# Kernel optimization log

Measured on AMD Instinct MI355X. Metric: run time of the kernel, lower is better.

Reference implementation:

```python
import jax, jax.numpy as jnp
import numpy as np

B, S, D = 4, 4096, 1024
E, H, TOPK = 8, 2752, 2


def setup_inputs() -> dict:
    key = jax.random.key(0)
    k0, k1, k2, k3, k4 = jax.random.split(key, 5)
    x = jax.random.normal(k0, (B, S, D), dtype=jnp.float32)
    gate_w = jax.random.normal(k1, (E, D), dtype=jnp.float32) * 0.02
    w1 = jax.random.normal(k2, (E, H, D), dtype=jnp.float32) * 0.02
    w2 = jax.random.normal(k3, (E, D, H), dtype=jnp.float32) * 0.02
    w3 = jax.random.normal(k4, (E, H, D), dtype=jnp.float32) * 0.02
    return {"x": x, "gate_w": gate_w, "w1": w1, "w2": w2, "w3": w3}


def reference(x, gate_w, w1, w2, w3):
    """MoE layer: softmax router -> top-k (normalized) -> per-expert SwiGLU FFN -> weighted combine."""
    b, s, d = x.shape
    xt = x.reshape(-1, d)                       # [T, D], T = B*S
    logits = xt @ gate_w.T                      # [T, E]
    scores = jax.nn.softmax(logits, axis=-1)
    topk_w, topk_i = jax.lax.top_k(scores, TOPK)  # [T, K]
    topk_w = topk_w / (jnp.sum(topk_w, axis=-1, keepdims=True) + 1e-20)

    y = jnp.zeros_like(xt)
    n_experts = gate_w.shape[0]
    for e in range(n_experts):
        # combine weight for expert e per token (0 if not routed to e)
        we = jnp.sum(jnp.where(topk_i == e, topk_w, 0.0), axis=-1)  # [T]
        h = jax.nn.silu(xt @ w1[e].T) * (xt @ w3[e].T)              # [T, H]
        y = y + we[:, None] * (h @ w2[e].T)                         # [T, D]
    return y.reshape(b, s, d)
```

## Files before the change

kernel.cpp:

```cpp
#include <hip/hip_runtime.h>
#include <hip/hip_bf16.h>
#include <stdint.h>

#define T_TOK 16384
#define D_DIM 1024
#define E_NUM 8
#define H_DIM 2752
#define NSLOT (T_TOK * 2)

typedef __bf16 bf16x8_t __attribute__((ext_vector_type(8)));
typedef float f32x4_t __attribute__((ext_vector_type(4)));
typedef float f32x16_t __attribute__((ext_vector_type(16)));

__device__ __forceinline__ uint16_t f2bf(float f) {
    union { float f; uint32_t u; } v; v.f = f;
    return (uint16_t)((v.u + 0x7FFFu + ((v.u >> 16) & 1u)) >> 16);
}
__device__ __forceinline__ ushort4 f4_to_bf4(float4 v) {
    ushort4 r; r.x = f2bf(v.x); r.y = f2bf(v.y); r.z = f2bf(v.z); r.w = f2bf(v.w);
    return r;
}
__device__ __forceinline__ void gl_lds16(const uint16_t* g, uint16_t* l) {
    __builtin_amdgcn_global_load_lds((const __attribute__((address_space(1))) void*)g,
                                     (__attribute__((address_space(3))) void*)l,
                                     16, 0, 0);
}

__global__ __launch_bounds__(256) void router_kernel(
    const float* __restrict__ x, const float* __restrict__ gw,
    int* __restrict__ topk_i, float* __restrict__ topk_w,
    uint16_t* __restrict__ Xb) {
    int tid = threadIdx.x;
    int t = blockIdx.x * 4 + (tid >> 6);
    int lane = tid & 63;
    const float* xr = x + (size_t)t * D_DIM;
    double acc[E_NUM];
#pragma unroll
    for (int e = 0; e < E_NUM; ++e) acc[e] = 0.0;
    for (int k = lane; k < D_DIM; k += 64) {
        double xv = (double)xr[k];
#pragma unroll
        for (int e = 0; e < E_NUM; ++e) acc[e] += xv * (double)gw[e * D_DIM + k];
    }
    {
        const float4* x4 = (const float4*)xr;
        ushort4* b4 = (ushort4*)(Xb + (size_t)t * D_DIM);
#pragma unroll
        for (int j = 0; j < 4; ++j) b4[lane + j * 64] = f4_to_bf4(x4[lane + j * 64]);
    }
#pragma unroll
    for (int e = 0; e < E_NUM; ++e) {
        double v = acc[e];
        for (int off = 32; off > 0; off >>= 1) v += __shfl_down(v, off, 64);
        acc[e] = v;
    }
    if (lane == 0) {
        int i0 = 0; double m0 = acc[0];
#pragma unroll
        for (int e = 1; e < E_NUM; ++e) if (acc[e] > m0) { m0 = acc[e]; i0 = e; }
        int i1 = -1; double m1 = -1.0e300;
#pragma unroll
        for (int e = 0; e < E_NUM; ++e) if (e != i0 && acc[e] > m1) { m1 = acc[e]; i1 = e; }
        double e1 = exp(m1 - m0);
        double s = 1.0 + e1;
        topk_i[t * 2 + 0] = i0; topk_i[t * 2 + 1] = i1;
        topk_w[t * 2 + 0] = (float)(1.0 / s);
        topk_w[t * 2 + 1] = (float)(e1 / s);
    }
}

__global__ __launch_bounds__(256) void count_kernel(
    const int* __restrict__ topk_i,
    int* __restrict__ counts_f, int* __restrict__ counts_s) {
    __shared__ int hf[E_NUM], hs[E_NUM];
    int tid = threadIdx.x;
    if (tid < E_NUM) { hf[tid] = 0; hs[tid] = 0; }
    __syncthreads();
    int t = blockIdx.x * 256 + tid;
    atomicAdd(&hf[topk_i[t * 2 + 0]], 1);
    atomicAdd(&hs[topk_i[t * 2 + 1]], 1);
    __syncthreads();
    if (tid < E_NUM) {
        if (hf[tid]) atomicAdd(&counts_f[tid], hf[tid]);
    } else if (tid < 2 * E_NUM) {
        int e = tid - E_NUM;
        if (hs[e]) atomicAdd(&counts_s[e], hs[e]);
    }
}

__global__ void prefix_kernel(const int* __restrict__ cf, const int* __restrict__ cs,
                              int* __restrict__ bases, int* __restrict__ splits,
                              int* __restrict__ cnts) {
    int s = 0;
    for (int e = 0; e < E_NUM; ++e) {
        bases[e] = s;
        splits[e] = s + cf[e];
        cnts[e] = cf[e] + cs[e];
        s += cnts[e];
    }
}

__global__ __launch_bounds__(256) void assign_kernel(
    const int* __restrict__ topk_i, const float* __restrict__ topk_w,
    const int* __restrict__ bases, const int* __restrict__ splits,
    int* __restrict__ fills_f, int* __restrict__ fills_s,
    int* __restrict__ slot_tok, float* __restrict__ slot_w) {
    __shared__ int hf[E_NUM], hs[E_NUM], bf[E_NUM], bs[E_NUM];
    int tid = threadIdx.x;
    if (tid < E_NUM) { hf[tid] = 0; hs[tid] = 0; }
    __syncthreads();
    int t = blockIdx.x * 256 + tid;
    int e0 = topk_i[t * 2 + 0], e1 = topk_i[t * 2 + 1];
    int r0 = atomicAdd(&hf[e0], 1);
    int r1 = atomicAdd(&hs[e1], 1);
    __syncthreads();
    if (tid < E_NUM) {
        bf[tid] = hf[tid] ? atomicAdd(&fills_f[tid], hf[tid]) : 0;
    } else if (tid < 2 * E_NUM) {
        int e = tid - E_NUM;
        bs[e] = hs[e] ? atomicAdd(&fills_s[e], hs[e]) : 0;
    }
    __syncthreads();
    int s0 = bases[e0] + bf[e0] + r0;
    int s1 = splits[e1] + bs[e1] + r1;
    slot_tok[s0] = t; slot_w[s0] = topk_w[t * 2 + 0];
    slot_tok[s1] = t; slot_w[s1] = topk_w[t * 2 + 1];
}

__global__ __launch_bounds__(256) void cvt13g_kernel(const float* __restrict__ w1,
                                                     const float* __restrict__ w3,
                                                     uint16_t* __restrict__ w1be,
                                                     uint16_t* __restrict__ w3be, int g) {
    size_t i = (size_t)blockIdx.x * 256 + threadIdx.x;
    size_t off = (size_t)g * 4 * H_DIM * D_DIM / 4;
    ((ushort4*)w1be)[i] = f4_to_bf4(((const float4*)w1)[off + i]);
    ((ushort4*)w3be)[i] = f4_to_bf4(((const float4*)w3)[off + i]);
}
__global__ __launch_bounds__(256) void cvt2_kernel(const float* __restrict__ w2,
                                                   uint16_t* __restrict__ w2b) {
    size_t i = (size_t)blockIdx.x * 256 + threadIdx.x;
    ((ushort4*)w2b)[i] = f4_to_bf4(((const float4*)w2)[i]);
}


__global__ __launch_bounds__(256) void gemm1_kernel(
    const uint16_t* __restrict__ Xb, const uint16_t* __restrict__ w1be,
    const uint16_t* __restrict__ w3be, const int* __restrict__ slot_tok,
    const int* __restrict__ cnts, const int* __restrict__ bases,
    uint16_t* __restrict__ hidden, int g) {
    int ez = blockIdx.z;
    int e = g * 4 + ez;
    int cnt = cnts[e];
    int m0 = blockIdx.y * 128;
    if (m0 >= cnt) return;
    int n0 = blockIdx.x * 64;
    int base = bases[e];
    const uint16_t* w1p = w1be + (size_t)ez * H_DIM * D_DIM;
    const uint16_t* w3p = w3be + (size_t)ez * H_DIM * D_DIM;

    __shared__ __align__(16) uint16_t As[128 * 64];
    __shared__ __align__(16) uint16_t B1s[64 * 64];
    __shared__ __align__(16) uint16_t B3s[64 * 64];

    int tid = threadIdx.x;
    int w = tid >> 6, lane = tid & 63;
    int l31 = lane & 31, khi = lane >> 5;
    int r8 = lane >> 3;
    int srcc = (lane & 7) ^ ((w * 4 + (lane >> 4)) & 7);
    int xr2 = (l31 >> 1) & 7;

    const uint16_t *pA0, *pA1, *pA2, *pA3, *pB1, *pB3;
    {
        int sr = w * 8 + r8;
        int t0 = slot_tok[base + min(m0 + 0 * 32 + sr, cnt - 1)];
        int t1 = slot_tok[base + min(m0 + 1 * 32 + sr, cnt - 1)];
        int t2 = slot_tok[base + min(m0 + 2 * 32 + sr, cnt - 1)];
        int t3 = slot_tok[base + min(m0 + 3 * 32 + sr, cnt - 1)];
        pA0 = Xb + (size_t)t0 * D_DIM + srcc * 8;
        pA1 = Xb + (size_t)t1 * D_DIM + srcc * 8;
        pA2 = Xb + (size_t)t2 * D_DIM + srcc * 8;
        pA3 = Xb + (size_t)t3 * D_DIM + srcc * 8;
        pB1 = w1p + (size_t)(n0 + sr) * D_DIM + srcc * 8;
        pB3 = w3p + (size_t)(n0 + sr) * D_DIM + srcc * 8;
    }
    uint16_t* lA = &As[(w * 8) * 64];
    uint16_t* lB1 = &B1s[(w * 8) * 64];
    uint16_t* lB3 = &B3s[(w * 8) * 64];

    f32x16_t acc1[2], acc3[2];
#pragma unroll
    for (int nf = 0; nf < 2; ++nf)
#pragma unroll
        for (int q = 0; q < 16; ++q) { acc1[nf][q] = 0.f; acc3[nf][q] = 0.f; }

    for (int k0 = 0; k0 < D_DIM; k0 += 64) {
        __syncthreads();
        gl_lds16(pA0, lA);
        gl_lds16(pA1, lA + 32 * 64);
        gl_lds16(pA2, lA + 64 * 64);
        gl_lds16(pA3, lA + 96 * 64);
        gl_lds16(pB1, lB1);
        gl_lds16(pB1 + 32 * D_DIM, lB1 + 32 * 64);
        gl_lds16(pB3, lB3);
        gl_lds16(pB3 + 32 * D_DIM, lB3 + 32 * 64);
        pA0 += 64; pA1 += 64; pA2 += 64; pA3 += 64; pB1 += 64; pB3 += 64;
        __syncthreads();

#pragma unroll
        for (int ks = 0; ks < 4; ++ks) {
            int ca = ((ks * 2 + khi) ^ xr2) * 8;
            bf16x8_t a0  = *(const bf16x8_t*)&As[(w * 32 + l31) * 64 + ca];
            bf16x8_t b1l = *(const bf16x8_t*)&B1s[l31 * 64 + ca];
            bf16x8_t b1h = *(const bf16x8_t*)&B1s[(32 + l31) * 64 + ca];
            bf16x8_t b3l = *(const bf16x8_t*)&B3s[l31 * 64 + ca];
            bf16x8_t b3h = *(const bf16x8_t*)&B3s[(32 + l31) * 64 + ca];
            acc1[0] = __builtin_amdgcn_mfma_f32_32x32x16_bf16(a0, b1l, acc1[0], 0, 0, 0);
            acc1[1] = __builtin_amdgcn_mfma_f32_32x32x16_bf16(a0, b1h, acc1[1], 0, 0, 0);
            acc3[0] = __builtin_amdgcn_mfma_f32_32x32x16_bf16(a0, b3l, acc3[0], 0, 0, 0);
            acc3[1] = __builtin_amdgcn_mfma_f32_32x32x16_bf16(a0, b3h, acc3[1], 0, 0, 0);
        }
    }

    {
        int rbase = m0 + w * 32 + 4 * khi;
#pragma unroll
        for (int reg = 0; reg < 16; ++reg) {
            int mrow = rbase + (reg & 3) + 8 * (reg >> 2);
            if (mrow < cnt) {
                size_t ro = (size_t)(base + mrow) * H_DIM + n0 + l31;
#pragma unroll
                for (int nf = 0; nf < 2; ++nf) {
                    float gv = acc1[nf][reg];
                    float s = gv / (1.0f + __expf(-gv));
                    float h = s * acc3[nf][reg];
                    hidden[ro + nf * 32] = f2bf(h);
                }
            }
        }
    }
}

__global__ __launch_bounds__(256) void gemm2_kernel(
    const uint16_t* __restrict__ hidden, const uint16_t* __restrict__ w2b,
    const int* __restrict__ cnts, const int* __restrict__ bases,
    const int* __restrict__ slot_tok, const float* __restrict__ slot_w,
    float* __restrict__ out) {
    int e = blockIdx.z;
    int cnt = cnts[e];
    int lin = blockIdx.y * 8 + blockIdx.x;
    int c8 = lin & 7, j = lin >> 3;
    int m_t = (j >> 3) * 8 + c8;
    int x_t = j & 7;
    int m0 = m_t * 128;
    if (m0 >= cnt) return;
    int base = bases[e];
    int d0 = x_t * 128;

    __shared__ __align__(16) uint16_t As[128 * 64];
    __shared__ __align__(16) uint16_t Bs[128 * 64];

    int tid = threadIdx.x;
    int w = tid >> 6, lane = tid & 63;
    int l31 = lane & 31, khi = lane >> 5;
    int r8 = lane >> 3;
    int srcc = (lane & 7) ^ ((w * 4 + (lane >> 4)) & 7);
    int xr2 = (l31 >> 1) & 7;
    int mh = w & 1, nh = w >> 1;

    const uint16_t *pA0, *pA1, *pA2, *pA3, *pB;
    {
        int sr = w * 8 + r8;
        int s0 = base + min(m0 + 0 * 32 + sr, cnt - 1);
        int s1 = base + min(m0 + 1 * 32 + sr, cnt - 1);
        int s2 = base + min(m0 + 2 * 32 + sr, cnt - 1);
        int s3 = base + min(m0 + 3 * 32 + sr, cnt - 1);
        pA0 = hidden + (size_t)s0 * H_DIM + srcc * 8;
        pA1 = hidden + (size_t)s1 * H_DIM + srcc * 8;
        pA2 = hidden + (size_t)s2 * H_DIM + srcc * 8;
        pA3 = hidden + (size_t)s3 * H_DIM + srcc * 8;
        pB = w2b + (size_t)(e * D_DIM + d0 + sr) * H_DIM + srcc * 8;
    }
    uint16_t* lA = &As[(w * 8) * 64];
    uint16_t* lB = &Bs[(w * 8) * 64];

    f32x16_t acc[2][2];
#pragma unroll
    for (int mf = 0; mf < 2; ++mf)
#pragma unroll
        for (int nf = 0; nf < 2; ++nf)
#pragma unroll
            for (int q = 0; q < 16; ++q) acc[mf][nf][q] = 0.f;

    for (int k0 = 0; k0 < H_DIM; k0 += 64) {
        __syncthreads();
        gl_lds16(pA0, lA);
        gl_lds16(pA1, lA + 32 * 64);
        gl_lds16(pA2, lA + 64 * 64);
        gl_lds16(pA3, lA + 96 * 64);
        gl_lds16(pB, lB);
        gl_lds16(pB + 32 * H_DIM, lB + 32 * 64);
        gl_lds16(pB + 64 * H_DIM, lB + 64 * 64);
        gl_lds16(pB + 96 * H_DIM, lB + 96 * 64);
        pA0 += 64; pA1 += 64; pA2 += 64; pA3 += 64; pB += 64;
        __syncthreads();

#pragma unroll
        for (int ks = 0; ks < 4; ++ks) {
            int ca = ((ks * 2 + khi) ^ xr2) * 8;
            bf16x8_t a0 = *(const bf16x8_t*)&As[(mh * 64 + l31) * 64 + ca];
            bf16x8_t a1 = *(const bf16x8_t*)&As[(mh * 64 + 32 + l31) * 64 + ca];
            bf16x8_t b0 = *(const bf16x8_t*)&Bs[(nh * 64 + l31) * 64 + ca];
            bf16x8_t b1 = *(const bf16x8_t*)&Bs[(nh * 64 + 32 + l31) * 64 + ca];
            acc[0][0] = __builtin_amdgcn_mfma_f32_32x32x16_bf16(a0, b0, acc[0][0], 0, 0, 0);
            acc[0][1] = __builtin_amdgcn_mfma_f32_32x32x16_bf16(a0, b1, acc[0][1], 0, 0, 0);
            acc[1][0] = __builtin_amdgcn_mfma_f32_32x32x16_bf16(a1, b0, acc[1][0], 0, 0, 0);
            acc[1][1] = __builtin_amdgcn_mfma_f32_32x32x16_bf16(a1, b1, acc[1][1], 0, 0, 0);
        }
    }

#pragma unroll
    for (int mf = 0; mf < 2; ++mf) {
        int rbase = m0 + mh * 64 + mf * 32 + 4 * khi;
#pragma unroll
        for (int reg = 0; reg < 16; ++reg) {
            int mr = rbase + (reg & 3) + 8 * (reg >> 2);
            if (mr < cnt) {
                int slot = base + mr;
                float wgt = slot_w[slot];
                int tok = slot_tok[slot];
                float* yr = out + (size_t)tok * D_DIM + d0 + nh * 64 + l31;
#pragma unroll
                for (int nf = 0; nf < 2; ++nf)
                    atomicAdd(&yr[nf * 32], wgt * acc[mf][nf][reg]);
            }
        }
    }
}

extern "C" void kernel_launch(void* const* d_in, const int* in_sizes, int n_in,
                              void* d_out, int out_size, void* d_ws, size_t ws_size,
                              hipStream_t stream) {
    const float* x  = (const float*)d_in[0];
    const float* gw = (const float*)d_in[1];
    const float* w1 = (const float*)d_in[2];
    const float* w2 = (const float*)d_in[3];
    const float* w3 = (const float*)d_in[4];
    float* out = (float*)d_out;
    char* ws = (char*)d_ws;

    int*   counts_f = (int*)(ws + 0);
    int*   counts_s = (int*)(ws + 256);
    int*   fills_f  = (int*)(ws + 512);
    int*   fills_s  = (int*)(ws + 768);
    int*   bases    = (int*)(ws + 1024);
    int*   splits   = (int*)(ws + 1280);
    int*   cnts     = (int*)(ws + 1536);
    int*   topk_i   = (int*)(ws + 4096);
    float* topk_w   = (float*)(ws + 4096 + 1 * 131072);
    int*   slot_tok = (int*)(ws + 4096 + 2 * 131072);
    float* slot_w   = (float*)(ws + 4096 + 3 * 131072);

    const size_t HID_OFF = 4ull << 20;
    const size_t W_OFF   = HID_OFF + (size_t)NSLOT * H_DIM * 2;
    const size_t W1SZ    = (size_t)H_DIM * D_DIM * 2;
    uint16_t* hidden = (uint16_t*)(ws + HID_OFF);
    uint16_t* w1be   = (uint16_t*)(ws + W_OFF);
    uint16_t* w3be   = (uint16_t*)(ws + W_OFF + 4 * W1SZ);
    uint16_t* w2b    = (uint16_t*)(ws + W_OFF);
    uint16_t* Xb     = (uint16_t*)d_out;

    hipMemsetAsync(ws, 0, 1024, stream);

    router_kernel<<<T_TOK / 4, 256, 0, stream>>>(x, gw, topk_i, topk_w, Xb);
    count_kernel<<<T_TOK / 256, 256, 0, stream>>>(topk_i, counts_f, counts_s);
    prefix_kernel<<<1, 1, 0, stream>>>(counts_f, counts_s, bases, splits, cnts);
    assign_kernel<<<T_TOK / 256, 256, 0, stream>>>(topk_i, topk_w, bases, splits,
                                                   fills_f, fills_s, slot_tok, slot_w);

    for (int g = 0; g < 2; ++g) {
        cvt13g_kernel<<<H_DIM * 4, 256, 0, stream>>>(w1, w3, w1be, w3be, g);
        gemm1_kernel<<<dim3(H_DIM / 64, 128, 4), 256, 0, stream>>>(
            Xb, w1be, w3be, slot_tok, cnts, bases, hidden, g);
    }

    hipMemsetAsync(out, 0, (size_t)T_TOK * D_DIM * sizeof(float), stream);
    cvt2_kernel<<<E_NUM * D_DIM * H_DIM / 1024, 256, 0, stream>>>(w2, w2b);
    gemm2_kernel<<<dim3(8, 128, E_NUM), 256, 0, stream>>>(
        hidden, w2b, cnts, bases, slot_tok, slot_w, out);
}
```

Baseline: 1.162 ms.

## Double-buffer LDS tiles in gemm2 to overlap global loads with MFMA

Gives the down-projection GEMM kernel two LDS buffers for the A and B tiles. It issues the next k-tile's global-to-LDS loads before computing on the current one, and uses vmcnt waits plus raw s_barriers in place of the two __syncthreads per iteration. The aim is to hide global load latency behind MFMA work. It doubles LDS use to 64KB per block, which may reduce occupancy, and the hand-written waitcnt and barriers rely on the LDS-DMA ordering being correct.

```diff
diff --git a/kernel.cpp b/kernel.cpp
--- a/kernel.cpp
+++ b/kernel.cpp
@@ -256,8 +256,8 @@
     int base = bases[e];
     int d0 = x_t * 128;
 
-    __shared__ __align__(16) uint16_t As[128 * 64];
-    __shared__ __align__(16) uint16_t Bs[128 * 64];
+    __shared__ __align__(16) uint16_t As[2][128 * 64];
+    __shared__ __align__(16) uint16_t Bs[2][128 * 64];
 
     int tid = threadIdx.x;
     int w = tid >> 6, lane = tid & 63;
@@ -280,8 +280,19 @@
         pA3 = hidden + (size_t)s3 * H_DIM + srcc * 8;
         pB = w2b + (size_t)(e * D_DIM + d0 + sr) * H_DIM + srcc * 8;
     }
-    uint16_t* lA = &As[(w * 8) * 64];
-    uint16_t* lB = &Bs[(w * 8) * 64];
+
+#define G2_STAGE(bi) do {                                          \
+        uint16_t* lA = &As[bi][(w * 8) * 64];                      \
+        uint16_t* lB = &Bs[bi][(w * 8) * 64];                      \
+        gl_lds16(pA0, lA);                                         \
+        gl_lds16(pA1, lA + 32 * 64);                               \
+        gl_lds16(pA2, lA + 64 * 64);                               \
+        gl_lds16(pA3, lA + 96 * 64);                               \
+        gl_lds16(pB, lB);                                          \
+        gl_lds16(pB + 32 * H_DIM, lB + 32 * 64);                   \
+        gl_lds16(pB + 64 * H_DIM, lB + 64 * 64);                   \
+        gl_lds16(pB + 96 * H_DIM, lB + 96 * 64);                   \
+        pA0 += 64; pA1 += 64; pA2 += 64; pA3 += 64; pB += 64; } while (0)
 
     f32x16_t acc[2][2];
 #pragma unroll
@@ -291,32 +302,34 @@
 #pragma unroll
             for (int q = 0; q < 16; ++q) acc[mf][nf][q] = 0.f;
 
-    for (int k0 = 0; k0 < H_DIM; k0 += 64) {
-        __syncthreads();
-        gl_lds16(pA0, lA);
-        gl_lds16(pA1, lA + 32 * 64);
-        gl_lds16(pA2, lA + 64 * 64);
-        gl_lds16(pA3, lA + 96 * 64);
-        gl_lds16(pB, lB);
-        gl_lds16(pB + 32 * H_DIM, lB + 32 * 64);
-        gl_lds16(pB + 64 * H_DIM, lB + 64 * 64);
-        gl_lds16(pB + 96 * H_DIM, lB + 96 * 64);
-        pA0 += 64; pA1 += 64; pA2 += 64; pA3 += 64; pB += 64;
-        __syncthreads();
-
+    G2_STAGE(0);
+    for (int t = 0; t < 43; ++t) {
+        int cur = t & 1;
+        if (t < 42) {
+            G2_STAGE(cur ^ 1);
+            asm volatile("s_waitcnt vmcnt(8)" ::: "memory");
+        } else {
+            asm volatile("s_waitcnt vmcnt(0)" ::: "memory");
+        }
+        __builtin_amdgcn_s_barrier();
+
+        const uint16_t* A = As[cur];
+        const uint16_t* B = Bs[cur];
 #pragma unroll
         for (int ks = 0; ks < 4; ++ks) {
             int ca = ((ks * 2 + khi) ^ xr2) * 8;
-            bf16x8_t a0 = *(const bf16x8_t*)&As[(mh * 64 + l31) * 64 + ca];
-            bf16x8_t a1 = *(const bf16x8_t*)&As[(mh * 64 + 32 + l31) * 64 + ca];
-            bf16x8_t b0 = *(const bf16x8_t*)&Bs[(nh * 64 + l31) * 64 + ca];
-            bf16x8_t b1 = *(const bf16x8_t*)&Bs[(nh * 64 + 32 + l31) * 64 + ca];
+            bf16x8_t a0 = *(const bf16x8_t*)&A[(mh * 64 + l31) * 64 + ca];
+            bf16x8_t a1 = *(const bf16x8_t*)&A[(mh * 64 + 32 + l31) * 64 + ca];
+            bf16x8_t b0 = *(const bf16x8_t*)&B[(nh * 64 + l31) * 64 + ca];
+            bf16x8_t b1 = *(const bf16x8_t*)&B[(nh * 64 + 32 + l31) * 64 + ca];
             acc[0][0] = __builtin_amdgcn_mfma_f32_32x32x16_bf16(a0, b0, acc[0][0], 0, 0, 0);
             acc[0][1] = __builtin_amdgcn_mfma_f32_32x32x16_bf16(a0, b1, acc[0][1], 0, 0, 0);
             acc[1][0] = __builtin_amdgcn_mfma_f32_32x32x16_bf16(a1, b0, acc[1][0], 0, 0, 0);
             acc[1][1] = __builtin_amdgcn_mfma_f32_32x32x16_bf16(a1, b1, acc[1][1], 0, 0, 0);
         }
-    }
+        __builtin_amdgcn_s_barrier();
+    }
+#undef G2_STAGE
 
 #pragma unroll
     for (int mf = 0; mf < 2; ++mf) {
```

New measurement: 1.160 ms. About the same (-0.1%).
